# Optimization experiments

Measured on AMD Instinct MI355X. Metric: run time of the kernel, lower is better.

## Reference

```python
import jax, jax.numpy as jnp
import numpy as np

N, E = 50000, 800000
C, A_ALL, RAD_IN, FC1, FC2 = 128, 256, 32, 64, 64
H, AH, VH = 8, 16, 16  # heads, alpha channels/head, value channels/head


def _radial_mlp(x, w1, b1, w2, b2, w3, b3):
    x = jax.nn.silu(x @ w1 + b1)
    x = jax.nn.silu(x @ w2 + b2)
    return x @ w3 + b3


def _smooth_leaky_relu(x, a=0.2):
    # Equiformer SmoothLeakyReLU: 0.5*(1+a)*x + 0.5*(1-a)*x*(2*sigmoid(x)-1)
    return 0.5 * (1.0 + a) * x + 0.5 * (1.0 - a) * x * (2.0 * jax.nn.sigmoid(x) - 1.0)


def _segment_softmax(scores, seg, num_segments):
    m = jax.ops.segment_max(scores, seg, num_segments=num_segments)
    m = jnp.where(jnp.isfinite(m), m, 0.0)
    e = jnp.exp(scores - m[seg])
    s = jax.ops.segment_sum(e, seg, num_segments=num_segments)
    return e / (s[seg] + 1e-16)


def setup_inputs():
    key = jax.random.key(0)
    ks = jax.random.split(key, 16)

    def g(k, shape):
        scale = 1.0 / np.sqrt(shape[0])
        return jax.random.normal(k, shape, dtype=jnp.float32) * scale

    return {
        "node_input": jax.random.normal(ks[0], (N, C), dtype=jnp.float32),
        "node_attr": jnp.ones((N, 1), jnp.float32),
        "edge_attr": jax.random.uniform(ks[1], (E, 1), dtype=jnp.float32),
        "edge_scalars": jax.random.normal(ks[2], (E, RAD_IN), dtype=jnp.float32),
        "edge_src": jax.random.randint(ks[3], (E,), 0, N, dtype=jnp.int32),
        "edge_dst": jax.random.randint(ks[4], (E,), 0, N, dtype=jnp.int32),
        "batch": jnp.zeros((N,), jnp.int32),
        "w_src": g(ks[5], (C, C)), "b_src": jnp.zeros((C,), jnp.float32),
        "w_dst": g(ks[6], (C, C)),
        "fc_w1": g(ks[7], (RAD_IN, FC1)), "fc_b1": jnp.zeros((FC1,), jnp.float32),
        "fc_w2": g(ks[8], (FC1, FC2)), "fc_b2": jnp.zeros((FC2,), jnp.float32),
        "fc_w3": g(ks[9], (FC2, C)), "fc_b3": jnp.zeros((C,), jnp.float32),
        "w_sep": g(ks[10], (C, A_ALL)), "b_sep": jnp.zeros((A_ALL,), jnp.float32),
        "alpha_dot": jax.random.normal(ks[11], (1, H, AH), dtype=jnp.float32) * np.sqrt(2.0 / (H * AH)),
        "w_proj": g(ks[12], (H * VH, C)), "b_proj": jnp.zeros((C,), jnp.float32),
    }


def reference(node_input, node_attr, edge_attr, edge_scalars, edge_src, edge_dst, batch,
              w_src, b_src, w_dst, fc_w1, fc_b1, fc_w2, fc_b2, fc_w3, fc_b3,
              w_sep, b_sep, alpha_dot, w_proj, b_proj):
    n_nodes = node_input.shape[0]
    n_edges = edge_src.shape[0]
    # merge_src / merge_dst (LinearRS; bias only on src)
    msg_src = node_input @ w_src + b_src                     # [N, C]
    msg_dst = node_input @ w_dst                             # [N, C]
    message = msg_src[edge_src] + msg_dst[edge_dst]          # [E, C] edge gather
    # SeparableFCTP: radial-weighted depthwise tensor product (scalar irreps)
    rad_w = _radial_mlp(edge_scalars, fc_w1, fc_b1, fc_w2, fc_b2, fc_w3, fc_b3)  # [E, C]
    message = message * edge_attr * rad_w                    # depthwise TP
    message = message @ w_sep + b_sep                        # [E, A_ALL] linear to attn_all
    # Vec2AttnHeads + split alpha/value per head
    msg_h = message.reshape(n_edges, H, AH + VH)
    alpha = _smooth_leaky_relu(msg_h[:, :, :AH])             # [E, H, AH]
    value = msg_h[:, :, AH:]                                 # [E, H, VH]
    score = jnp.einsum('ehk,ahk->eh', alpha, alpha_dot)      # [E, H]
    att = _segment_softmax(score, edge_dst, n_nodes)[..., None]
    out = jax.ops.segment_sum(value * att, edge_dst, num_segments=n_nodes)  # scatter-add
    out = out.reshape(n_nodes, H * VH)                       # AttnHeads2Vec
    return out @ w_proj + b_proj
```

## Files before the change

### kernel.cpp

```cpp
#include <hip/hip_runtime.h>

#define NN 50000
#define NE 800000

typedef unsigned short u16;
typedef __bf16 bf16x8 __attribute__((ext_vector_type(8)));
typedef float f32x4 __attribute__((ext_vector_type(4)));

__device__ __forceinline__ u16 f2b(float f){
  unsigned x = __float_as_uint(f);
  return (u16)((x + 0x7FFFu + ((x>>16)&1u)) >> 16);
}
#define MFMA16(a,b,c) __builtin_amdgcn_mfma_f32_16x16x32_bf16((a),(b),(c),0,0,0)

__global__ void k_prep(const float* __restrict__ w1, const float* __restrict__ w2,
                       const float* __restrict__ w3, const float* __restrict__ wsep,
                       const float* __restrict__ wsrc, const float* __restrict__ wdst,
                       const float* __restrict__ wproj,
                       u16* __restrict__ w1T, u16* __restrict__ w2T,
                       u16* __restrict__ w3T, u16* __restrict__ wsepT,
                       u16* __restrict__ wsrcT, u16* __restrict__ wdstT,
                       u16* __restrict__ wprojT)
{
  int id = blockIdx.x*256 + threadIdx.x;
  if (id < 2048)  { int n=id>>5,  k=id&31;  w1T[id]   = f2b(w1[k*64+n]);    return; } id -= 2048;
  if (id < 4096)  { int n=id>>6,  k=id&63;  w2T[id]   = f2b(w2[k*64+n]);    return; } id -= 4096;
  if (id < 8192)  { int n=id>>6,  k=id&63;  w3T[id]   = f2b(w3[k*128+n]);   return; } id -= 8192;
  if (id < 32768) { int n=id>>7,  k=id&127; wsepT[id] = f2b(wsep[k*256+n]); return; } id -= 32768;
  if (id < 16384) { int n=id>>7,  k=id&127; wsrcT[id] = f2b(wsrc[k*128+n]); return; } id -= 16384;
  if (id < 16384) { int n=id>>7,  k=id&127; wdstT[id] = f2b(wdst[k*128+n]); return; } id -= 16384;
  if (id < 16384) { int n=id>>7,  k=id&127; wprojT[id]= f2b(wproj[k*128+n]); return; }
}

__launch_bounds__(256)
__global__ void k_node(const float* __restrict__ x, const u16* __restrict__ wsrcT,
                       const u16* __restrict__ wdstT, const float* __restrict__ bsrc,
                       float* __restrict__ msgsrc, float* __restrict__ msgdst)
{
  __shared__ u16 sX[64*136];
  __shared__ u16 sW[128*136];
  __shared__ float sB[128];
  const int tid = threadIdx.x;
  const int n0 = blockIdx.x*64;
  for (int idx = tid; idx < 64*32; idx += 256){
    int r = idx>>5, s = idx&31;
    float4 v = make_float4(0.f,0.f,0.f,0.f);
    if (n0 + r < NN) v = *(const float4*)(x + (size_t)(n0+r)*128 + s*4);
    ushort4 o; o.x=f2b(v.x); o.y=f2b(v.y); o.z=f2b(v.z); o.w=f2b(v.w);
    *(ushort4*)(&sX[r*136 + s*4]) = o;
  }
  const int wave = tid>>6, lane = tid&63, l15 = lane&15, q = lane>>4;
  for (int half = 0; half < 2; ++half){
    const u16* wT = half ? wdstT : wsrcT;
    for (int idx = tid; idx < 128*16; idx += 256){
      int r = idx>>4, s = idx&15;
      *(uint4*)(&sW[r*136 + s*8]) = *(const uint4*)(wT + r*128 + s*8);
    }
    if (tid < 128) sB[tid] = half ? 0.0f : bsrc[tid];
    __syncthreads();
    f32x4 acc[8];
    #pragma unroll
    for (int n=0;n<8;++n) acc[n] = (f32x4){0.f,0.f,0.f,0.f};
    #pragma unroll
    for (int k0=0;k0<128;k0+=32){
      bf16x8 a = *(const bf16x8*)(&sX[(wave*16+l15)*136 + k0 + q*8]);
      #pragma unroll
      for (int n=0;n<8;++n){
        bf16x8 b = *(const bf16x8*)(&sW[(n*16+l15)*136 + k0 + q*8]);
        acc[n] = MFMA16(a,b,acc[n]);
      }
    }
    float* outp = half ? msgdst : msgsrc;
    #pragma unroll
    for (int n=0;n<8;++n){
      #pragma unroll
      for (int r=0;r<4;++r){
        int row = n0 + wave*16 + q*4 + r;
        if (row < NN) outp[(size_t)row*128 + n*16 + l15] = acc[n][r] + sB[n*16+l15];
      }
    }
    __syncthreads();
  }
}

#define PM 136
#define PH 72
#define PX 40
__launch_bounds__(256)
__global__ void k_edge(const float* __restrict__ escal, const float* __restrict__ eattr,
                       const int* __restrict__ esrc, const int* __restrict__ edst,
                       const float* __restrict__ msgsrc, const float* __restrict__ msgdst,
                       const u16* __restrict__ w1T, const u16* __restrict__ w2T,
                       const u16* __restrict__ w3T, const u16* __restrict__ wsepT,
                       const float* __restrict__ b1, const float* __restrict__ b2,
                       const float* __restrict__ b3, const float* __restrict__ bsep,
                       const float* __restrict__ adot,
                       float* __restrict__ num, float* __restrict__ denom)
{
  __shared__ __attribute__((aligned(16))) char pool[49408];
  u16*   sXs  = (u16*)(pool + 0);
  u16*   sW1  = (u16*)(pool + 5120);
  u16*   sW2  = (u16*)(pool + 10240);
  u16*   sH1  = (u16*)(pool + 19456);
  u16*   sMsg = (u16*)(pool + 28672);
  float* sB1  = (float*)(pool + 46080);
  float* sB2  = (float*)(pool + 46336);
  float* sB3  = (float*)(pool + 46592);
  float* sBs  = (float*)(pool + 47104);
  float* sAD  = (float*)(pool + 48128);
  float* sEA  = (float*)(pool + 48640);
  int*   sSrc = (int*)(pool + 48896);
  int*   sDst = (int*)(pool + 49152);
  u16*   sH2  = (u16*)(pool + 0);
  u16*   sW3C = (u16*)(pool + 10240);
  u16*   sWsp = (u16*)(pool + 10240);

  const int tid = threadIdx.x;
  const int e0 = blockIdx.x*64;
  const int wave = tid>>6, lane = tid&63, l15 = lane&15, q = lane>>4;

  {
    for (int j = tid; j < 512; j += 256){ int r=j>>3, s=j&7;
      float4 v = *(const float4*)(escal + (size_t)(e0+r)*32 + s*4);
      ushort4 o; o.x=f2b(v.x); o.y=f2b(v.y); o.z=f2b(v.z); o.w=f2b(v.w);
      *(ushort4*)&sXs[r*PX + s*4] = o; }
    if (tid < 256){ int r=tid>>2, s=tid&3;
      *(uint4*)&sW1[r*PX + s*8] = *(const uint4*)(w1T + r*32 + s*8); }
    for (int j = tid; j < 512; j += 256){ int r=j>>3, s=j&7;
      *(uint4*)&sW2[r*PH + s*8] = *(const uint4*)(w2T + r*64 + s*8); }
    if (tid < 64)  sB1[tid] = b1[tid];
    if (tid < 64)  sB2[tid] = b2[tid];
    if (tid < 128) sB3[tid] = b3[tid];
    sBs[tid] = bsep[tid];
    if (tid < 128) sAD[tid] = adot[tid];
    if (tid < 64){ sEA[tid] = eattr[e0+tid]; sSrc[tid] = esrc[e0+tid]; sDst[tid] = edst[e0+tid]; }
  }
  __syncthreads();

  {
    f32x4 acc[4];
    #pragma unroll
    for (int n=0;n<4;++n) acc[n] = (f32x4){0.f,0.f,0.f,0.f};
    bf16x8 a = *(const bf16x8*)&sXs[(wave*16+l15)*PX + q*8];
    #pragma unroll
    for (int n=0;n<4;++n){
      bf16x8 b = *(const bf16x8*)&sW1[(n*16+l15)*PX + q*8];
      acc[n] = MFMA16(a,b,acc[n]);
    }
    #pragma unroll
    for (int n=0;n<4;++n){
      #pragma unroll
      for (int r=0;r<4;++r){
        float v = acc[n][r] + sB1[n*16+l15];
        float h = v / (1.0f + __expf(-v));
        sH1[(wave*16+q*4+r)*PH + n*16+l15] = f2b(h);
      }
    }
  }
  __syncthreads();

  {
    f32x4 acc[4];
    #pragma unroll
    for (int n=0;n<4;++n) acc[n] = (f32x4){0.f,0.f,0.f,0.f};
    #pragma unroll
    for (int k0=0;k0<64;k0+=32){
      bf16x8 a = *(const bf16x8*)&sH1[(wave*16+l15)*PH + k0 + q*8];
      #pragma unroll
      for (int n=0;n<4;++n){
        bf16x8 b = *(const bf16x8*)&sW2[(n*16+l15)*PH + k0 + q*8];
        acc[n] = MFMA16(a,b,acc[n]);
      }
    }
    #pragma unroll
    for (int n=0;n<4;++n){
      #pragma unroll
      for (int r=0;r<4;++r){
        float v = acc[n][r] + sB2[n*16+l15];
        float h = v / (1.0f + __expf(-v));
        sH2[(wave*16+q*4+r)*PH + n*16+l15] = f2b(h);
      }
    }
  }
  __syncthreads();

  for (int ch=0; ch<2; ++ch){
    for (int j = tid; j < 512; j += 256){ int r=j>>3, s=j&7;
      *(uint4*)&sW3C[r*PH + s*8] = *(const uint4*)(w3T + (size_t)(ch*64+r)*64 + s*8); }
    __syncthreads();
    const int m0 = (wave&1)*2, n0 = (wave>>1)*2;
    f32x4 acc[2][2];
    #pragma unroll
    for (int mm=0;mm<2;++mm)
      #pragma unroll
      for (int nn=0;nn<2;++nn) acc[mm][nn] = (f32x4){0.f,0.f,0.f,0.f};
    #pragma unroll
    for (int k0=0;k0<64;k0+=32){
      bf16x8 a0 = *(const bf16x8*)&sH2[((m0  )*16+l15)*PH + k0 + q*8];
      bf16x8 a1 = *(const bf16x8*)&sH2[((m0+1)*16+l15)*PH + k0 + q*8];
      bf16x8 b0 = *(const bf16x8*)&sW3C[((n0  )*16+l15)*PH + k0 + q*8];
      bf16x8 b1 = *(const bf16x8*)&sW3C[((n0+1)*16+l15)*PH + k0 + q*8];
      acc[0][0] = MFMA16(a0,b0,acc[0][0]);
      acc[1][0] = MFMA16(a1,b0,acc[1][0]);
      acc[0][1] = MFMA16(a0,b1,acc[0][1]);
      acc[1][1] = MFMA16(a1,b1,acc[1][1]);
    }
    #pragma unroll
    for (int mm=0;mm<2;++mm){
      #pragma unroll
      for (int nn=0;nn<2;++nn){
        int c = ch*64 + (n0+nn)*16 + l15;
        #pragma unroll
        for (int r=0;r<4;++r){
          float v = acc[mm][nn][r] + sB3[c];
          sMsg[((m0+mm)*16+q*4+r)*PM + c] = f2b(v);
        }
      }
    }
    __syncthreads();
  }

  for (int idx = tid; idx < 64*32; idx += 256){
    int r = idx>>5, s = idx&31;
    int cs = s*4;
    float4 a4 = *(const float4*)(msgsrc + (size_t)sSrc[r]*128 + cs);
    float4 d4 = *(const float4*)(msgdst + (size_t)sDst[r]*128 + cs);
    float ea = sEA[r];
    ushort4 rw = *(ushort4*)&sMsg[r*PM + cs];
    ushort4 o;
    o.x = f2b((a4.x + d4.x) * ea * __uint_as_float(((unsigned)rw.x)<<16));
    o.y = f2b((a4.y + d4.y) * ea * __uint_as_float(((unsigned)rw.y)<<16));
    o.z = f2b((a4.z + d4.z) * ea * __uint_as_float(((unsigned)rw.z)<<16));
    o.w = f2b((a4.w + d4.w) * ea * __uint_as_float(((unsigned)rw.w)<<16));
    *(ushort4*)&sMsg[r*PM + cs] = o;
  }
  __syncthreads();

  const int fm0 = (wave&1)*2, fn0 = (wave>>1)*2;
  for (int ch=0; ch<4; ++ch){
    for (int j = tid; j < 1024; j += 256){ int r=j>>4, s=j&15;
      *(uint4*)&sWsp[r*PM + s*8] = *(const uint4*)(wsepT + (size_t)(ch*64+r)*128 + s*8); }
    __syncthreads();
    f32x4 acc[2][2];
    #pragma unroll
    for (int mm=0;mm<2;++mm)
      #pragma unroll
      for (int nn=0;nn<2;++nn) acc[mm][nn] = (f32x4){0.f,0.f,0.f,0.f};
    #pragma unroll
    for (int k0=0;k0<128;k0+=32){
      bf16x8 a0 = *(const bf16x8*)&sMsg[((fm0  )*16+l15)*PM + k0 + q*8];
      bf16x8 a1 = *(const bf16x8*)&sMsg[((fm0+1)*16+l15)*PM + k0 + q*8];
      bf16x8 b0 = *(const bf16x8*)&sWsp[((fn0  )*16+l15)*PM + k0 + q*8];
      bf16x8 b1 = *(const bf16x8*)&sWsp[((fn0+1)*16+l15)*PM + k0 + q*8];
      acc[0][0] = MFMA16(a0,b0,acc[0][0]);
      acc[1][0] = MFMA16(a1,b0,acc[1][0]);
      acc[0][1] = MFMA16(a0,b1,acc[0][1]);
      acc[1][1] = MFMA16(a1,b1,acc[1][1]);
    }
    {
      const int h  = ch*2 + (fn0>>1);
      const int ca = ch*64 + fn0*16;
      const float ba = sBs[ca + l15];
      const float bv = sBs[ca + 16 + l15];
      const float ad = sAD[h*16 + l15];
      #pragma unroll
      for (int mm=0;mm<2;++mm){
        #pragma unroll
        for (int r=0;r<4;++r){
          int eloc = (fm0+mm)*16 + q*4 + r;
          float av  = acc[mm][0][r] + ba;
          float sig = 1.0f/(1.0f + __expf(-av));
          float sl  = av*(0.2f + 0.8f*sig);
          float contrib = sl * ad;
          contrib += __shfl_xor(contrib, 1);
          contrib += __shfl_xor(contrib, 2);
          contrib += __shfl_xor(contrib, 4);
          contrib += __shfl_xor(contrib, 8);
          float w  = __expf(contrib);
          int dst  = sDst[eloc];
          float vv = acc[mm][1][r] + bv;
          unsafeAtomicAdd(&num[(size_t)dst*128 + h*16 + l15], w*vv);
          if (l15 == 0) unsafeAtomicAdd(&denom[(size_t)dst*8 + h], w);
        }
      }
    }
    __syncthreads();
  }
}

__launch_bounds__(256)
__global__ void k_out(const float* __restrict__ num, const float* __restrict__ denom,
                      const u16* __restrict__ wprojT, const float* __restrict__ bproj,
                      float* __restrict__ out)
{
  __shared__ u16 sX[64*136];
  __shared__ u16 sW[128*136];
  __shared__ float sB[128];
  const int tid = threadIdx.x;
  const int n0 = blockIdx.x*64;
  for (int idx = tid; idx < 64*128; idx += 256){
    int r = idx>>7, c = idx&127;
    float xv = 0.f;
    int row = n0 + r;
    if (row < NN){
      float d = denom[row*8 + (c>>4)];
      xv = num[(size_t)row*128 + c] / (d + 1e-16f);
    }
    sX[r*136 + c] = f2b(xv);
  }
  for (int idx = tid; idx < 128*16; idx += 256){ int r=idx>>4, s=idx&15;
    *(uint4*)&sW[r*136 + s*8] = *(const uint4*)(wprojT + r*128 + s*8); }
  if (tid < 128) sB[tid] = bproj[tid];
  __syncthreads();
  const int wave = tid>>6, lane = tid&63, l15 = lane&15, q = lane>>4;
  f32x4 acc[8];
  #pragma unroll
  for (int n=0;n<8;++n) acc[n] = (f32x4){0.f,0.f,0.f,0.f};
  #pragma unroll
  for (int k0=0;k0<128;k0+=32){
    bf16x8 a = *(const bf16x8*)&sX[(wave*16+l15)*136 + k0 + q*8];
    #pragma unroll
    for (int n=0;n<8;++n){
      bf16x8 b = *(const bf16x8*)&sW[(n*16+l15)*136 + k0 + q*8];
      acc[n] = MFMA16(a,b,acc[n]);
    }
  }
  #pragma unroll
  for (int n=0;n<8;++n){
    #pragma unroll
    for (int r=0;r<4;++r){
      int row = n0 + wave*16 + q*4 + r;
      if (row < NN) out[(size_t)row*128 + n*16 + l15] = acc[n][r] + sB[n*16+l15];
    }
  }
}

extern "C" void kernel_launch(void* const* d_in, const int* in_sizes, int n_in,
                              void* d_out, int out_size, void* d_ws, size_t ws_size,
                              hipStream_t stream)
{
  const float* node_input = (const float*)d_in[0];
  const float* eattr = (const float*)d_in[2];
  const float* escal = (const float*)d_in[3];
  const int*   esrc  = (const int*)d_in[4];
  const int*   edst  = (const int*)d_in[5];
  const float* wsrc  = (const float*)d_in[7];
  const float* bsrc  = (const float*)d_in[8];
  const float* wdst  = (const float*)d_in[9];
  const float* w1    = (const float*)d_in[10];
  const float* b1    = (const float*)d_in[11];
  const float* w2    = (const float*)d_in[12];
  const float* b2    = (const float*)d_in[13];
  const float* w3    = (const float*)d_in[14];
  const float* b3    = (const float*)d_in[15];
  const float* wsep  = (const float*)d_in[16];
  const float* bsep  = (const float*)d_in[17];
  const float* adot  = (const float*)d_in[18];
  const float* wproj = (const float*)d_in[19];
  const float* bproj = (const float*)d_in[20];

  char* ws = (char*)d_ws;
  size_t off = 0;
  auto alloc = [&](size_t bytes)->void*{ void* p = ws + off; off += (bytes + 255) & ~(size_t)255; return p; };
  float* msgsrc = (float*)alloc((size_t)NN*128*4);
  float* msgdst = (float*)alloc((size_t)NN*128*4);
  float* num    = (float*)alloc((size_t)NN*128*4);
  float* denom  = (float*)alloc((size_t)NN*8*4);
  u16* w1T    = (u16*)alloc(2048*2);
  u16* w2T    = (u16*)alloc(4096*2);
  u16* w3T    = (u16*)alloc(8192*2);
  u16* wsepT  = (u16*)alloc(32768*2);
  u16* wsrcT  = (u16*)alloc(16384*2);
  u16* wdstT  = (u16*)alloc(16384*2);
  u16* wprojT = (u16*)alloc(16384*2);

  hipMemsetAsync(num,   0, (size_t)NN*128*4, stream);
  hipMemsetAsync(denom, 0, (size_t)NN*8*4,   stream);

  k_prep<<<376, 256, 0, stream>>>(w1,w2,w3,wsep,wsrc,wdst,wproj,
                                  w1T,w2T,w3T,wsepT,wsrcT,wdstT,wprojT);
  k_node<<<782, 256, 0, stream>>>(node_input, wsrcT, wdstT, bsrc, msgsrc, msgdst);
  k_edge<<<12500, 256, 0, stream>>>(escal, eattr, esrc, edst, msgsrc, msgdst,
                                    w1T, w2T, w3T, wsepT, b1, b2, b3, bsep, adot,
                                    num, denom);
  k_out<<<782, 256, 0, stream>>>(num, denom, wprojT, bproj, (float*)d_out);
}
```

Before: 914.6 us.

## Sort edges by destination and pre-reduce segment contributions before atomics

Adds a counting sort of edges by destination (histogram, single-block scan, atomic scatter) so each edge block processes edges grouped by destination node. Inside the edge kernel, per-chunk weighted values and weights are staged in shared memory and summed per destination segment before the global atomic adds, cutting atomic traffic. It also prefetches the next wsep chunk while the reduction runs. The cost is three extra kernels, including a serial one-block scan, plus indirect gathers of edge scalars and attributes through the permutation.

```diff
diff --git a/kernel.cpp b/kernel.cpp
--- a/kernel.cpp
+++ b/kernel.cpp
@@ -1,4 +1,5 @@
 #include <hip/hip_runtime.h>
+
 
 #define NN 50000
 #define NE 800000
@@ -32,6 +33,36 @@
   if (id < 16384) { int n=id>>7,  k=id&127; wprojT[id]= f2b(wproj[k*128+n]); return; }
 }
 
+__global__ void k_hist(const int* __restrict__ edst, int* __restrict__ counts){
+  int e = blockIdx.x*256 + threadIdx.x;
+  if (e < NE) atomicAdd(&counts[edst[e]], 1);
+}
+
+__launch_bounds__(256)
+__global__ void k_scan(const int* __restrict__ counts, int* __restrict__ cursor){
+  __shared__ int ssum[256];
+  const int t = threadIdx.x;
+  const int base = t*196;
+  int s = 0;
+  for (int i=0;i<196;++i){ int j=base+i; if (j<NN) s += counts[j]; }
+  ssum[t] = s; __syncthreads();
+  if (t==0){ int run=0; for (int i=0;i<256;++i){ int v=ssum[i]; ssum[i]=run; run+=v; } }
+  __syncthreads();
+  int run = ssum[t];
+  for (int i=0;i<196;++i){ int j=base+i;
+    if (j<NN){ cursor[j]=run; run += counts[j]; } }
+}
+
+__global__ void k_scatter(const int* __restrict__ esrc, const int* __restrict__ edst,
+                          int* __restrict__ cursor, int* __restrict__ sEid,
+                          int* __restrict__ sSrcA, int* __restrict__ sDstA){
+  int e = blockIdx.x*256 + threadIdx.x;
+  if (e >= NE) return;
+  int d = edst[e];
+  int pos = atomicAdd(&cursor[d], 1);
+  sEid[pos] = e; sDstA[pos] = d; sSrcA[pos] = esrc[e];
+}
+
 __launch_bounds__(256)
 __global__ void k_node(const float* __restrict__ x, const u16* __restrict__ wsrcT,
                        const u16* __restrict__ wdstT, const float* __restrict__ bsrc,
@@ -88,7 +119,8 @@
 #define PX 40
 __launch_bounds__(256)
 __global__ void k_edge(const float* __restrict__ escal, const float* __restrict__ eattr,
-                       const int* __restrict__ esrc, const int* __restrict__ edst,
+                       const int* __restrict__ sEid, const int* __restrict__ sSrcA,
+                       const int* __restrict__ sDstA,
                        const float* __restrict__ msgsrc, const float* __restrict__ msgdst,
                        const u16* __restrict__ w1T, const u16* __restrict__ w2T,
                        const u16* __restrict__ w3T, const u16* __restrict__ wsepT,
@@ -97,7 +129,7 @@
                        const float* __restrict__ adot,
                        float* __restrict__ num, float* __restrict__ denom)
 {
-  __shared__ __attribute__((aligned(16))) char pool[49408];
+  __shared__ __attribute__((aligned(16))) char pool[49920];
   u16*   sXs  = (u16*)(pool + 0);
   u16*   sW1  = (u16*)(pool + 5120);
   u16*   sW2  = (u16*)(pool + 10240);
@@ -111,9 +143,14 @@
   float* sEA  = (float*)(pool + 48640);
   int*   sSrc = (int*)(pool + 48896);
   int*   sDst = (int*)(pool + 49152);
+  int*   sSegDst   = (int*)(pool + 49408);
+  u16*   sSegStart = (u16*)(pool + 49664);
+  int*   sNseg     = (int*)(pool + 49796);
   u16*   sH2  = (u16*)(pool + 0);
   u16*   sW3C = (u16*)(pool + 10240);
   u16*   sWsp = (u16*)(pool + 10240);
+  float* sNumT= (float*)(pool + 0);
+  float* sWt  = (float*)(pool + 9216);
 
   const int tid = threadIdx.x;
   const int e0 = blockIdx.x*64;
@@ -121,7 +158,8 @@
 
   {
     for (int j = tid; j < 512; j += 256){ int r=j>>3, s=j&7;
-      float4 v = *(const float4*)(escal + (size_t)(e0+r)*32 + s*4);
+      int eid = sEid[e0+r];
+      float4 v = *(const float4*)(escal + (size_t)eid*32 + s*4);
       ushort4 o; o.x=f2b(v.x); o.y=f2b(v.y); o.z=f2b(v.z); o.w=f2b(v.w);
       *(ushort4*)&sXs[r*PX + s*4] = o; }
     if (tid < 256){ int r=tid>>2, s=tid&3;
@@ -133,9 +171,18 @@
     if (tid < 128) sB3[tid] = b3[tid];
     sBs[tid] = bsep[tid];
     if (tid < 128) sAD[tid] = adot[tid];
-    if (tid < 64){ sEA[tid] = eattr[e0+tid]; sSrc[tid] = esrc[e0+tid]; sDst[tid] = edst[e0+tid]; }
-  }
-  __syncthreads();
+    if (tid < 64){ int p=e0+tid; sEA[tid] = eattr[sEid[p]];
+                   sSrc[tid] = sSrcA[p]; sDst[tid] = sDstA[p]; }
+  }
+  __syncthreads();
+
+  if (tid == 0){
+    int ns = 0;
+    for (int r=0;r<64;++r){
+      if (r==0 || sDst[r]!=sDst[r-1]){ sSegDst[ns]=sDst[r]; sSegStart[ns]=(u16)r; ++ns; }
+    }
+    sSegStart[ns] = 64; sNseg[0] = ns;
+  }
 
   {
     f32x4 acc[4];
@@ -234,13 +281,15 @@
     o.w = f2b((a4.w + d4.w) * ea * __uint_as_float(((unsigned)rw.w)<<16));
     *(ushort4*)&sMsg[r*PM + cs] = o;
   }
-  __syncthreads();
 
   const int fm0 = (wave&1)*2, fn0 = (wave>>1)*2;
+  const int hh  = fn0>>1;
+  __syncthreads();
+  for (int j = tid; j < 1024; j += 256){ int r=j>>4, s=j&15;
+    *(uint4*)&sWsp[r*PM + s*8] = *(const uint4*)(wsepT + (size_t)r*128 + s*8); }
+  __syncthreads();
+
   for (int ch=0; ch<4; ++ch){
-    for (int j = tid; j < 1024; j += 256){ int r=j>>4, s=j&15;
-      *(uint4*)&sWsp[r*PM + s*8] = *(const uint4*)(wsepT + (size_t)(ch*64+r)*128 + s*8); }
-    __syncthreads();
     f32x4 acc[2][2];
     #pragma unroll
     for (int mm=0;mm<2;++mm)
@@ -258,16 +307,15 @@
       acc[1][1] = MFMA16(a1,b1,acc[1][1]);
     }
     {
-      const int h  = ch*2 + (fn0>>1);
       const int ca = ch*64 + fn0*16;
       const float ba = sBs[ca + l15];
       const float bv = sBs[ca + 16 + l15];
-      const float ad = sAD[h*16 + l15];
+      const float ad = sAD[(ch*2+hh)*16 + l15];
       #pragma unroll
       for (int mm=0;mm<2;++mm){
         #pragma unroll
         for (int r=0;r<4;++r){
-          int eloc = (fm0+mm)*16 + q*4 + r;
+          int row = (fm0+mm)*16 + q*4 + r;
           float av  = acc[mm][0][r] + ba;
           float sig = 1.0f/(1.0f + __expf(-av));
           float sl  = av*(0.2f + 0.8f*sig);
@@ -277,14 +325,36 @@
           contrib += __shfl_xor(contrib, 4);
           contrib += __shfl_xor(contrib, 8);
           float w  = __expf(contrib);
-          int dst  = sDst[eloc];
           float vv = acc[mm][1][r] + bv;
-          unsafeAtomicAdd(&num[(size_t)dst*128 + h*16 + l15], w*vv);
-          if (l15 == 0) unsafeAtomicAdd(&denom[(size_t)dst*8 + h], w);
+          sNumT[row*36 + hh*16 + l15] = w*vv;
+          if (l15 == 0) sWt[row*2 + hh] = w;
         }
       }
     }
     __syncthreads();
+    if (ch < 3){
+      for (int j = tid; j < 1024; j += 256){ int r=j>>4, s=j&15;
+        *(uint4*)&sWsp[r*PM + s*8] = *(const uint4*)(wsepT + (size_t)((ch+1)*64+r)*128 + s*8); }
+    }
+    {
+      int ns = sNseg[0];
+      for (int wk = tid; wk < ns*32; wk += 256){
+        int s = wk>>5, c = wk&31;
+        int beg = sSegStart[s], end = sSegStart[s+1];
+        float a0 = 0.f;
+        for (int r=beg;r<end;++r) a0 += sNumT[r*36 + c];
+        int h = ch*2 + (c>>4);
+        unsafeAtomicAdd(&num[(size_t)sSegDst[s]*128 + h*16 + (c&15)], a0);
+      }
+      for (int wk = tid; wk < ns*2; wk += 256){
+        int s = wk>>1, hx = wk&1;
+        int beg = sSegStart[s], end = sSegStart[s+1];
+        float a0 = 0.f;
+        for (int r=beg;r<end;++r) a0 += sWt[r*2 + hx];
+        unsafeAtomicAdd(&denom[(size_t)sSegDst[s]*8 + ch*2 + hx], a0);
+      }
+    }
+    if (ch < 3) __syncthreads();
   }
 }
 
@@ -366,6 +436,11 @@
   float* msgdst = (float*)alloc((size_t)NN*128*4);
   float* num    = (float*)alloc((size_t)NN*128*4);
   float* denom  = (float*)alloc((size_t)NN*8*4);
+  int* counts  = (int*)alloc((size_t)NN*4);
+  int* cursor  = (int*)alloc((size_t)NN*4);
+  int* sEid    = (int*)alloc((size_t)NE*4);
+  int* sSrcA   = (int*)alloc((size_t)NE*4);
+  int* sDstA   = (int*)alloc((size_t)NE*4);
   u16* w1T    = (u16*)alloc(2048*2);
   u16* w2T    = (u16*)alloc(4096*2);
   u16* w3T    = (u16*)alloc(8192*2);
@@ -374,13 +449,18 @@
   u16* wdstT  = (u16*)alloc(16384*2);
   u16* wprojT = (u16*)alloc(16384*2);
 
-  hipMemsetAsync(num,   0, (size_t)NN*128*4, stream);
-  hipMemsetAsync(denom, 0, (size_t)NN*8*4,   stream);
+  hipMemsetAsync(num,    0, (size_t)NN*128*4, stream);
+  hipMemsetAsync(denom,  0, (size_t)NN*8*4,   stream);
+  hipMemsetAsync(counts, 0, (size_t)NN*4,     stream);
 
   k_prep<<<376, 256, 0, stream>>>(w1,w2,w3,wsep,wsrc,wdst,wproj,
                                   w1T,w2T,w3T,wsepT,wsrcT,wdstT,wprojT);
+  k_hist<<<3125, 256, 0, stream>>>(edst, counts);
+  k_scan<<<1, 256, 0, stream>>>(counts, cursor);
+  k_scatter<<<3125, 256, 0, stream>>>(esrc, edst, cursor, sEid, sSrcA, sDstA);
   k_node<<<782, 256, 0, stream>>>(node_input, wsrcT, wdstT, bsrc, msgsrc, msgdst);
-  k_edge<<<12500, 256, 0, stream>>>(escal, eattr, esrc, edst, msgsrc, msgdst,
+  k_edge<<<12500, 256, 0, stream>>>(escal, eattr, sEid, sSrcA, sDstA,
+                                    msgsrc, msgdst,
                                     w1T, w2T, w3T, wsepT, b1, b2, b3, bsep, adot,
                                     num, denom);
   k_out<<<782, 256, 0, stream>>>(num, denom, wprojT, bproj, (float*)d_out);
```

After: 990.1 us. +8.3%, slower.
